# Performance work log

Hardware: AMD Instinct MI355X
Metric: run time of the kernel (lower is better)

Reference implementation:

```python
import jax, jax.numpy as jnp
import numpy as np

N, E = 50000, 800000
IN, HID, OUT = 128, 128, 64
H, ED = 4, 3
D = HID // H  # per-head dim = 32


def _w(key, shape):
    fan_in = shape[-1]
    return jax.random.normal(key, shape, dtype=jnp.float32) / np.sqrt(fan_in)


def setup_inputs() -> dict:
    key = jax.random.key(0)
    ks = jax.random.split(key, 32)
    inp = {
        "x": jax.random.normal(ks[0], (N, IN), dtype=jnp.float32),
        "edge_index": jax.random.randint(ks[1], (2, E), 0, N, dtype=jnp.int32),
        "edge_attr": jax.random.normal(ks[2], (E, ED), dtype=jnp.float32),
        # layer 1 TransformerConv (bias=False)
        "Wq1": _w(ks[3], (HID, IN)), "Wk1": _w(ks[4], (HID, IN)),
        "Wv1": _w(ks[5], (HID, IN)), "We1": _w(ks[6], (HID, ED)),
        "Ws1": _w(ks[7], (HID, IN)),
        # layer 1 MLP [HID,HID,HID]
        "M1a": _w(ks[8], (HID, HID)), "b1a": jnp.zeros((HID,), jnp.float32),
        "M1b": _w(ks[9], (HID, HID)), "b1b": jnp.zeros((HID,), jnp.float32),
        # layer 2 TransformerConv
        "Wq2": _w(ks[10], (HID, HID)), "Wk2": _w(ks[11], (HID, HID)),
        "Wv2": _w(ks[12], (HID, HID)), "We2": _w(ks[13], (HID, ED)),
        "Ws2": _w(ks[14], (HID, HID)),
        # layer 2 MLP
        "M2a": _w(ks[15], (HID, HID)), "b2a": jnp.zeros((HID,), jnp.float32),
        "M2b": _w(ks[16], (HID, HID)), "b2b": jnp.zeros((HID,), jnp.float32),
        # final MLP [HID,HID,OUT], plain_last=False
        "Wf1": _w(ks[17], (HID, HID)), "bf1": jnp.zeros((HID,), jnp.float32),
        "Wf2": _w(ks[18], (OUT, HID)), "bf2": jnp.zeros((OUT,), jnp.float32),
    }
    return inp


def _gelu(x):
    return jax.nn.gelu(x, approximate=True)


def _transformer_conv(x, src, dst, edge_attr, Wq, Wk, Wv, We, Ws, n_nodes):
    # PyG TransformerConv: x_j = x[src] (message source), x_i = x[dst] (target)
    q = (x @ Wq.T).reshape(n_nodes, H, D)
    e = (edge_attr @ We.T).reshape(-1, H, D)              # [E,H,D]
    k = (x @ Wk.T).reshape(n_nodes, H, D)[src] + e        # [E,H,D]
    v = (x @ Wv.T).reshape(n_nodes, H, D)[src] + e        # [E,H,D]
    alpha = jnp.einsum("ehd,ehd->eh", q[dst], k) / jnp.float32(np.sqrt(D))
    # segment softmax over incoming edges of each target node
    m = jax.ops.segment_max(alpha, dst, num_segments=n_nodes)  # [N,H]
    m = jnp.where(jnp.isfinite(m), m, 0.0)
    p = jnp.exp(alpha - m[dst])
    s = jax.ops.segment_sum(p, dst, num_segments=n_nodes)      # [N,H]
    a = p / jnp.maximum(s[dst], 1e-16)                         # [E,H]
    out = jax.ops.segment_sum(a[:, :, None] * v, dst, num_segments=n_nodes)
    out = out.reshape(n_nodes, H * D)
    # root_weight=True (default): skip connection through lin_skip (no bias)
    return out + x @ Ws.T


def _mlp2(x, Wa, ba, Wb, bb):
    # PyG MLP with plain_last=False: act after every linear, norm=None
    h = _gelu(x @ Wa.T + ba)
    return _gelu(h @ Wb.T + bb)


def reference(x, edge_index, edge_attr,
              Wq1, Wk1, Wv1, We1, Ws1, M1a, b1a, M1b, b1b,
              Wq2, Wk2, Wv2, We2, Ws2, M2a, b2a, M2b, b2b,
              Wf1, bf1, Wf2, bf2):
    n_nodes = x.shape[0]
    src, dst = edge_index[0], edge_index[1]
    h = _transformer_conv(x, src, dst, edge_attr, Wq1, Wk1, Wv1, We1, Ws1, n_nodes)
    h = h + _mlp2(h, M1a, b1a, M1b, b1b)
    h = _transformer_conv(h, src, dst, edge_attr, Wq2, Wk2, Wv2, We2, Ws2, n_nodes)
    h = h + _mlp2(h, M2a, b2a, M2b, b2b)
    return _mlp2(h, Wf1, bf1, Wf2, bf2)
```

## Files before the change

### kernel.cpp

```cpp
#include <hip/hip_runtime.h>
#include <hip/hip_bf16.h>
#include <math.h>

#define NN 50000
#define NE 800000
#define NPAD 50048
#define BCAP 48

typedef unsigned short u16;
typedef unsigned int u32;
typedef __attribute__((ext_vector_type(8))) short short8;
typedef __attribute__((ext_vector_type(4))) float float4v;

__device__ __forceinline__ float us2f(u16 u) { return __uint_as_float(((unsigned)u) << 16); }
__device__ __forceinline__ float blo(u32 u) { return __uint_as_float(u << 16); }
__device__ __forceinline__ float bhi(u32 u) { return __uint_as_float(u & 0xffff0000u); }
__device__ __forceinline__ u16 f2us(float f) {
    unsigned x = __float_as_uint(f);
    return (u16)((x + 0x7FFFu + ((x >> 16) & 1u)) >> 16);
}
__device__ __forceinline__ float gelu_f(float x) {
    float p = x * x;
    float t = x * fmaf(p, 0.0713548162726f, 1.5957691216057308f);
    float e = __expf(-t);
    return x * __builtin_amdgcn_rcpf(1.0f + e);
}
__device__ __forceinline__ void lds_fence() {
    asm volatile("s_waitcnt lgkmcnt(0)" ::: "memory");
}

__device__ __forceinline__ float4v mfma4p(const u16* __restrict__ WP, int tile, int l,
                                          short8 a0, short8 a1, short8 a2, short8 a3) {
    const short8* wp = (const short8*)WP + (size_t)tile * 256 + l;
    short8 b0 = wp[0], b1 = wp[64], b2 = wp[128], b3 = wp[192];
    float4v acc = {0.f, 0.f, 0.f, 0.f};
    acc = __builtin_amdgcn_mfma_f32_16x16x32_bf16(a0, b0, acc, 0, 0, 0);
    acc = __builtin_amdgcn_mfma_f32_16x16x32_bf16(a1, b1, acc, 0, 0, 0);
    acc = __builtin_amdgcn_mfma_f32_16x16x32_bf16(a2, b2, acc, 0, 0, 0);
    acc = __builtin_amdgcn_mfma_f32_16x16x32_bf16(a3, b3, acc, 0, 0, 0);
    return acc;
}


__global__ void k_scatter(const int* __restrict__ srcv, const int* __restrict__ dstv,
                          const float* __restrict__ eattr, int* __restrict__ cursor,
                          int4* __restrict__ rec) {
    int e = blockIdx.x * blockDim.x + threadIdx.x;
    if (e >= NE) return;
    int dst = dstv[e];
    int pos = atomicAdd(&cursor[dst], 1);
    if (pos >= BCAP) return;
    int4 r;
    r.x = srcv[e];
    r.y = __float_as_int(eattr[e * 3 + 0]);
    r.z = __float_as_int(eattr[e * 3 + 1]);
    r.w = __float_as_int(eattr[e * 3 + 2]);
    rec[(size_t)dst * BCAP + pos] = r;
}


struct CvtEnt { const float* s; u16* d; int n; float sc; };
struct CvtTab { CvtEnt e[14]; };
__global__ void k_cvt_w(CvtTab tab) {
    CvtEnt E = tab.e[blockIdx.x >> 3];
    int chunk = blockIdx.x & 7;
    int per = E.n >> 3;
    int lo = chunk * per, hi = lo + per;
    for (int o = lo + threadIdx.x; o < hi; o += blockDim.x) {
        int tile = o >> 11;
        int q = (o >> 9) & 3;
        int l = (o >> 3) & 63;
        int j = o & 7;
        int row = tile * 16 + (l & 15);
        int col = q * 32 + (l >> 4) * 8 + j;
        E.d[o] = f2us(E.s[row * 128 + col] * E.sc);
    }
}


__device__ __forceinline__ void stage_plain(u16* buf, int kb, int m, int tt, float4v acc) {
#pragma unroll
    for (int r = 0; r < 4; ++r) buf[(kb * 4 + r) * 136 + tt * 16 + m] = f2us(acc[r]);
}
__device__ __forceinline__ void store128(const u16* buf, u16* dst, int r0w, int coff, int l) {
#pragma unroll
    for (int it = 0; it < 4; ++it) {
        int j = it * 64 + l;
        int row = j >> 4, col = (j & 15) * 8;
        *(uint4*)(dst + (size_t)(r0w + row) * 512 + coff + col) = *(const uint4*)&buf[row * 136 + col];
    }
}
__device__ __forceinline__ void read_frags(const u16* buf, int m, int kb,
                                           short8& f0, short8& f1, short8& f2, short8& f3) {
    const u16* p = buf + m * 136 + kb * 8;
    f0 = *(const short8*)(p);
    f1 = *(const short8*)(p + 32);
    f2 = *(const short8*)(p + 64);
    f3 = *(const short8*)(p + 96);
}


__global__ __launch_bounds__(256, 4) void k_qkvs1(const float* __restrict__ Ain,
                                                  const u16* __restrict__ W,
                                                  u16* __restrict__ QKVS) {
    __shared__ u16 tile[4][16 * 136];
    int tid = threadIdx.x;
    int l = tid & 63, w = tid >> 6, m = l & 15, kb = l >> 4;
    int r0w = blockIdx.x * 64 + w * 16;
    u16* my = tile[w];

    short8 a0, a1, a2, a3;
    {
        const float* ap = Ain + (size_t)(r0w + m) * 128;
        bool ok = (r0w + m) < NN;
        short8* dsts[4] = {&a0, &a1, &a2, &a3};
#pragma unroll
        for (int i = 0; i < 4; ++i) {
            short8 r;
            if (ok) {
                const float* p = ap + (kb + i * 4) * 8;
                float4 f0 = *(const float4*)p;
                float4 f1 = *(const float4*)(p + 4);
                r[0]=(short)f2us(f0.x); r[1]=(short)f2us(f0.y); r[2]=(short)f2us(f0.z); r[3]=(short)f2us(f0.w);
                r[4]=(short)f2us(f1.x); r[5]=(short)f2us(f1.y); r[6]=(short)f2us(f1.z); r[7]=(short)f2us(f1.w);
            } else {
#pragma unroll
                for (int j = 0; j < 8; ++j) r[j] = 0;
            }
            *dsts[i] = r;
        }
    }

#pragma unroll
    for (int tt = 0; tt < 8; ++tt) stage_plain(my, kb, m, tt, mfma4p(W, tt, l, a0, a1, a2, a3));
    lds_fence();
    store128(my, QKVS, r0w, 0, l);
    lds_fence();
#pragma unroll
    for (int tt = 0; tt < 4; ++tt) {
        float4v acc = mfma4p(W, 8 + tt, l, a0, a1, a2, a3);
        int c = tt * 32 + 8 * (m >> 2) + (m & 3);
#pragma unroll
        for (int r = 0; r < 4; ++r) my[(kb * 4 + r) * 136 + c] = f2us(acc[r]);
    }
#pragma unroll
    for (int tt = 0; tt < 4; ++tt) {
        float4v acc = mfma4p(W, 16 + tt, l, a0, a1, a2, a3);
        int c = tt * 32 + 8 * (m >> 2) + (m & 3) + 4;
#pragma unroll
        for (int r = 0; r < 4; ++r) my[(kb * 4 + r) * 136 + c] = f2us(acc[r]);
    }
    lds_fence();
    store128(my, QKVS, r0w, 128, l);
    lds_fence();
#pragma unroll
    for (int tt = 0; tt < 4; ++tt) {
        float4v acc = mfma4p(W, 12 + tt, l, a0, a1, a2, a3);
        int c = tt * 32 + 8 * (m >> 2) + (m & 3);
#pragma unroll
        for (int r = 0; r < 4; ++r) my[(kb * 4 + r) * 136 + c] = f2us(acc[r]);
    }
#pragma unroll
    for (int tt = 0; tt < 4; ++tt) {
        float4v acc = mfma4p(W, 20 + tt, l, a0, a1, a2, a3);
        int c = tt * 32 + 8 * (m >> 2) + (m & 3) + 4;
#pragma unroll
        for (int r = 0; r < 4; ++r) my[(kb * 4 + r) * 136 + c] = f2us(acc[r]);
    }
    lds_fence();
    store128(my, QKVS, r0w, 256, l);
    lds_fence();
#pragma unroll
    for (int tt = 0; tt < 8; ++tt) stage_plain(my, kb, m, tt, mfma4p(W, 24 + tt, l, a0, a1, a2, a3));
    lds_fence();
    store128(my, QKVS, r0w, 384, l);
}


__global__ __launch_bounds__(256, 4) void k_mlp_qkvs(const u16* __restrict__ Ain,
                                                     const u16* __restrict__ Wm,
                                                     const float* __restrict__ bias1,
                                                     const float* __restrict__ bias2,
                                                     const u16* __restrict__ Wq,
                                                     u16* __restrict__ QKVS) {
    __shared__ u16 shb[4][16 * 136];
    __shared__ u16 t1b[4][16 * 136];
    int tid = threadIdx.x;
    int l = tid & 63, w = tid >> 6, m = l & 15, kb = l >> 4;
    int r0w = blockIdx.x * 64 + w * 16;
    u16* sh = shb[w];
    u16* t1 = t1b[w];

    const short8* arow = (const short8*)(Ain + (size_t)(r0w + m) * 128);
    short8 a0 = arow[kb], a1 = arow[kb + 4], a2 = arow[kb + 8], a3 = arow[kb + 12];
    {
        u16* p = sh + m * 136 + kb * 8;
        *(short8*)(p) = a0;
        *(short8*)(p + 32) = a1;
        *(short8*)(p + 64) = a2;
        *(short8*)(p + 96) = a3;
    }
#pragma unroll
    for (int tt = 0; tt < 8; ++tt) {
        float4v acc = mfma4p(Wm, tt, l, a0, a1, a2, a3);
        float bv = bias1[tt * 16 + m];
#pragma unroll
        for (int r = 0; r < 4; ++r)
            t1[(kb * 4 + r) * 136 + tt * 16 + m] = f2us(gelu_f(acc[r] + bv));
    }
    lds_fence();
    short8 c0, c1, c2, c3;
    read_frags(t1, m, kb, c0, c1, c2, c3);
#pragma unroll
    for (int tt = 0; tt < 8; ++tt) {
        float4v acc = mfma4p(Wm + 16384, tt, l, c0, c1, c2, c3);
        float bv = bias2[tt * 16 + m];
#pragma unroll
        for (int r = 0; r < 4; ++r) {
            int idx = (kb * 4 + r) * 136 + tt * 16 + m;
            sh[idx] = f2us(gelu_f(acc[r] + bv) + us2f(sh[idx]));
        }
    }
    lds_fence();
    short8 h0, h1, h2, h3;
    read_frags(sh, m, kb, h0, h1, h2, h3);

#pragma unroll
    for (int tt = 0; tt < 8; ++tt) stage_plain(t1, kb, m, tt, mfma4p(Wq, tt, l, h0, h1, h2, h3));
    lds_fence();
    store128(t1, QKVS, r0w, 0, l);
    lds_fence();
#pragma unroll
    for (int tt = 0; tt < 4; ++tt) {
        float4v acc = mfma4p(Wq, 8 + tt, l, h0, h1, h2, h3);
        int c = tt * 32 + 8 * (m >> 2) + (m & 3);
#pragma unroll
        for (int r = 0; r < 4; ++r) t1[(kb * 4 + r) * 136 + c] = f2us(acc[r]);
    }
#pragma unroll
    for (int tt = 0; tt < 4; ++tt) {
        float4v acc = mfma4p(Wq, 16 + tt, l, h0, h1, h2, h3);
        int c = tt * 32 + 8 * (m >> 2) + (m & 3) + 4;
#pragma unroll
        for (int r = 0; r < 4; ++r) t1[(kb * 4 + r) * 136 + c] = f2us(acc[r]);
    }
    lds_fence();
    store128(t1, QKVS, r0w, 128, l);
    lds_fence();
#pragma unroll
    for (int tt = 0; tt < 4; ++tt) {
        float4v acc = mfma4p(Wq, 12 + tt, l, h0, h1, h2, h3);
        int c = tt * 32 + 8 * (m >> 2) + (m & 3);
#pragma unroll
        for (int r = 0; r < 4; ++r) t1[(kb * 4 + r) * 136 + c] = f2us(acc[r]);
    }
#pragma unroll
    for (int tt = 0; tt < 4; ++tt) {
        float4v acc = mfma4p(Wq, 20 + tt, l, h0, h1, h2, h3);
        int c = tt * 32 + 8 * (m >> 2) + (m & 3) + 4;
#pragma unroll
        for (int r = 0; r < 4; ++r) t1[(kb * 4 + r) * 136 + c] = f2us(acc[r]);
    }
    lds_fence();
    store128(t1, QKVS, r0w, 256, l);
    lds_fence();
#pragma unroll
    for (int tt = 0; tt < 8; ++tt) stage_plain(t1, kb, m, tt, mfma4p(Wq, 24 + tt, l, h0, h1, h2, h3));
    lds_fence();
    store128(t1, QKVS, r0w, 384, l);
}


__global__ __launch_bounds__(256, 4) void k_mlp_final(const u16* __restrict__ Ain,
                                                      const u16* __restrict__ Wm,
                                                      const float* __restrict__ bias1,
                                                      const float* __restrict__ bias2,
                                                      const u16* __restrict__ Wf,
                                                      const float* __restrict__ bf1,
                                                      const float* __restrict__ bf2,
                                                      float* __restrict__ outp) {
    __shared__ u16 shb[4][16 * 136];
    __shared__ u16 t1b[4][16 * 136];
    int tid = threadIdx.x;
    int l = tid & 63, w = tid >> 6, m = l & 15, kb = l >> 4;
    int r0w = blockIdx.x * 64 + w * 16;
    u16* sh = shb[w];
    u16* t1 = t1b[w];

    const short8* arow = (const short8*)(Ain + (size_t)(r0w + m) * 128);
    short8 a0 = arow[kb], a1 = arow[kb + 4], a2 = arow[kb + 8], a3 = arow[kb + 12];
    {
        u16* p = sh + m * 136 + kb * 8;
        *(short8*)(p) = a0;
        *(short8*)(p + 32) = a1;
        *(short8*)(p + 64) = a2;
        *(short8*)(p + 96) = a3;
    }
#pragma unroll
    for (int tt = 0; tt < 8; ++tt) {
        float4v acc = mfma4p(Wm, tt, l, a0, a1, a2, a3);
        float bv = bias1[tt * 16 + m];
#pragma unroll
        for (int r = 0; r < 4; ++r)
            t1[(kb * 4 + r) * 136 + tt * 16 + m] = f2us(gelu_f(acc[r] + bv));
    }
    lds_fence();
    short8 c0, c1, c2, c3;
    read_frags(t1, m, kb, c0, c1, c2, c3);
#pragma unroll
    for (int tt = 0; tt < 8; ++tt) {
        float4v acc = mfma4p(Wm + 16384, tt, l, c0, c1, c2, c3);
        float bv = bias2[tt * 16 + m];
#pragma unroll
        for (int r = 0; r < 4; ++r) {
            int idx = (kb * 4 + r) * 136 + tt * 16 + m;
            sh[idx] = f2us(gelu_f(acc[r] + bv) + us2f(sh[idx]));
        }
    }
    lds_fence();
    short8 h0, h1, h2, h3;
    read_frags(sh, m, kb, h0, h1, h2, h3);
#pragma unroll
    for (int tt = 0; tt < 8; ++tt) {
        float4v acc = mfma4p(Wf, tt, l, h0, h1, h2, h3);
        float bv = bf1[tt * 16 + m];
#pragma unroll
        for (int r = 0; r < 4; ++r)
            t1[(kb * 4 + r) * 136 + tt * 16 + m] = f2us(gelu_f(acc[r] + bv));
    }
    lds_fence();
    short8 f0, f1, f2, f3;
    read_frags(t1, m, kb, f0, f1, f2, f3);
    lds_fence();
#pragma unroll
    for (int tt = 0; tt < 4; ++tt) {
        float4v acc = mfma4p(Wf + 16384, tt, l, f0, f1, f2, f3);
        float bv = bf2[tt * 16 + m];
#pragma unroll
        for (int r = 0; r < 4; ++r)
            t1[(kb * 4 + r) * 136 + tt * 16 + m] = f2us(gelu_f(acc[r] + bv));
    }
    lds_fence();
#pragma unroll
    for (int it = 0; it < 2; ++it) {
        int j = it * 64 + l;
        int row = j >> 3, col = (j & 7) * 8;
        int grow = r0w + row;
        if (grow < NN) {
            uint4 pk = *(const uint4*)&t1[row * 136 + col];
            const u16* pv = (const u16*)&pk;
            float* po = outp + (size_t)grow * 64 + col;
            float4 o0 = {us2f(pv[0]), us2f(pv[1]), us2f(pv[2]), us2f(pv[3])};
            float4 o1 = {us2f(pv[4]), us2f(pv[5]), us2f(pv[6]), us2f(pv[7])};
            *(float4*)po = o0;
            *(float4*)(po + 4) = o1;
        }
    }
}


__global__ __launch_bounds__(256) void k_conv(const int* __restrict__ cursor,
                                              const int4* __restrict__ rec,
                                              const u16* __restrict__ qkvs,
                                              const float* __restrict__ We,
                                              u16* __restrict__ out) {
    int n = blockIdx.x * 4 + (threadIdx.x >> 6);
    int l = threadIdx.x & 63;
    int half = l >> 5;
    int li = l & 31;
    int c0 = (li >> 3) * 32 + (li & 7) * 4;
    const u16* qrow = qkvs + (size_t)n * 512;
    uint2 qu = *(const uint2*)(qrow + c0);
    uint2 su = *(const uint2*)(qrow + 384 + c0);
    float q0 = blo(qu.x), q1 = bhi(qu.x), q2 = blo(qu.y), q3 = bhi(qu.y);
    float g0, g1, g2;
    {
        const float* wp = We + c0 * 3;
        g0 = fmaf(q3, wp[9],  fmaf(q2, wp[6], fmaf(q1, wp[3], q0 * wp[0])));
        g1 = fmaf(q3, wp[10], fmaf(q2, wp[7], fmaf(q1, wp[4], q0 * wp[1])));
        g2 = fmaf(q3, wp[11], fmaf(q2, wp[8], fmaf(q1, wp[5], q0 * wp[2])));
#pragma unroll
        for (int d = 1; d <= 4; d <<= 1) {
            g0 += __shfl_xor(g0, d);
            g1 += __shfl_xor(g1, d);
            g2 += __shfl_xor(g2, d);
        }
    }
    int cntall = min(cursor[n], BCAP);
    int base = n * BCAP;
    float ss = 0.f, o0 = 0.f, o1 = 0.f, o2 = 0.f, o3 = 0.f, S0 = 0.f, S1 = 0.f, S2 = 0.f;
    int kvoff = 128 + li * 8;

    auto edge = [&](int4 r, uint4 kv) {
        float part = fmaf(q3, bhi(kv.y), fmaf(q2, blo(kv.y), fmaf(q1, bhi(kv.x), q0 * blo(kv.x))));
        part += __shfl_xor(part, 1);
        part += __shfl_xor(part, 2);
        part += __shfl_xor(part, 4);
        float ea0 = __int_as_float(r.y), ea1 = __int_as_float(r.z), ea2 = __int_as_float(r.w);
        float alpha = fmaf(ea2, g2, fmaf(ea1, g1, fmaf(ea0, g0, part)));
        float p = __expf(fminf(alpha, 80.f));
        o0 = fmaf(p, blo(kv.z), o0);
        o1 = fmaf(p, bhi(kv.z), o1);
        o2 = fmaf(p, blo(kv.w), o2);
        o3 = fmaf(p, bhi(kv.w), o3);
        ss += p;
        S0 = fmaf(p, ea0, S0);
        S1 = fmaf(p, ea1, S1);
        S2 = fmaf(p, ea2, S2);
    };

    int e = base + half;
    int cnt = (half < cntall) ? ((cntall - half + 1) >> 1) : 0;
    if (cnt & 1) {
        int4 r = rec[e];
        uint4 kv = *(const uint4*)(qkvs + (size_t)r.x * 512 + kvoff);
        edge(r, kv);
        e += 2;
    }
    for (int i = 0; i < (cnt >> 1); ++i, e += 4) {
        int4 ra = rec[e], rb = rec[e + 2];
        uint4 kva = *(const uint4*)(qkvs + (size_t)ra.x * 512 + kvoff);
        uint4 kvb = *(const uint4*)(qkvs + (size_t)rb.x * 512 + kvoff);
        edge(ra, kva);
        edge(rb, kvb);
    }
    o0 += __shfl_xor(o0, 32);
    o1 += __shfl_xor(o1, 32);
    o2 += __shfl_xor(o2, 32);
    o3 += __shfl_xor(o3, 32);
    ss += __shfl_xor(ss, 32);
    S0 += __shfl_xor(S0, 32);
    S1 += __shfl_xor(S1, 32);
    S2 += __shfl_xor(S2, 32);
    if (half == 0) {
        float inv = __builtin_amdgcn_rcpf(fmaxf(ss, 1e-16f));
        const float* wp = We + c0 * 3;
        o0 = fmaf(wp[2],  S2, fmaf(wp[1],  S1, fmaf(wp[0], S0, o0)));
        o1 = fmaf(wp[5],  S2, fmaf(wp[4],  S1, fmaf(wp[3], S0, o1)));
        o2 = fmaf(wp[8],  S2, fmaf(wp[7],  S1, fmaf(wp[6], S0, o2)));
        o3 = fmaf(wp[11], S2, fmaf(wp[10], S1, fmaf(wp[9], S0, o3)));
        float r0v = fmaf(o0, inv, blo(su.x));
        float r1v = fmaf(o1, inv, bhi(su.x));
        float r2v = fmaf(o2, inv, blo(su.y));
        float r3v = fmaf(o3, inv, bhi(su.y));
        uint2 ou;
        ou.x = (u32)f2us(r0v) | ((u32)f2us(r1v) << 16);
        ou.y = (u32)f2us(r2v) | ((u32)f2us(r3v) << 16);
        *(uint2*)(out + (size_t)n * 128 + c0) = ou;
    }
}


extern "C" void kernel_launch(void* const* d_in, const int* in_sizes, int n_in,
                              void* d_out, int out_size, void* d_ws, size_t ws_size,
                              hipStream_t stream) {
    const float* x = (const float*)d_in[0];
    const int* ei = (const int*)d_in[1];
    const float* eattr = (const float*)d_in[2];
    const float* Wq1 = (const float*)d_in[3];
    const float* Wk1 = (const float*)d_in[4];
    const float* Wv1 = (const float*)d_in[5];
    const float* We1 = (const float*)d_in[6];
    const float* Ws1 = (const float*)d_in[7];
    const float* M1a = (const float*)d_in[8];
    const float* b1a = (const float*)d_in[9];
    const float* M1b = (const float*)d_in[10];
    const float* b1b = (const float*)d_in[11];
    const float* Wq2 = (const float*)d_in[12];
    const float* Wk2 = (const float*)d_in[13];
    const float* Wv2 = (const float*)d_in[14];
    const float* We2 = (const float*)d_in[15];
    const float* Ws2 = (const float*)d_in[16];
    const float* M2a = (const float*)d_in[17];
    const float* b2a = (const float*)d_in[18];
    const float* M2b = (const float*)d_in[19];
    const float* b2b = (const float*)d_in[20];
    const float* Wf1 = (const float*)d_in[21];
    const float* bf1 = (const float*)d_in[22];
    const float* Wf2 = (const float*)d_in[23];
    const float* bf2 = (const float*)d_in[24];

    char* ws = (char*)d_ws;
    size_t off = 0;
    auto alloc = [&](size_t bytes) -> void* {
        void* p = ws + off;
        off = (off + bytes + 255) & ~(size_t)255;
        return p;
    };
    int* cursor = (int*)alloc((size_t)NN * 4);
    int4* rec = (int4*)alloc((size_t)NN * BCAP * 16);
    u16* QKVS = (u16*)alloc((size_t)NPAD * 512 * 2);
    u16* Ha = (u16*)alloc((size_t)NPAD * 128 * 2);
    u16* WB[14];
    const int wsz[14] = {16384, 16384, 16384, 16384, 16384, 16384, 16384,
                         16384, 16384, 16384, 16384, 16384, 16384, 8192};
    for (int i = 0; i < 14; ++i) WB[i] = (u16*)alloc((size_t)wsz[i] * 2);

    const int* srcv = ei;
    const int* dstv = ei + NE;

    hipMemsetAsync(cursor, 0, (size_t)NN * 4, stream);
    k_scatter<<<(NE + 255) / 256, 256, 0, stream>>>(srcv, dstv, eattr, cursor, rec);

    CvtTab tab;
    const float* wsrc[14] = {Wq1, Wk1, Wv1, Ws1, Wq2, Wk2, Wv2, Ws2,
                             M1a, M1b, M2a, M2b, Wf1, Wf2};
    const float SC = 0.17677669529663687f;
    for (int i = 0; i < 14; ++i) {
        tab.e[i].s = wsrc[i];
        tab.e[i].d = WB[i];
        tab.e[i].n = wsz[i];
        tab.e[i].sc = (i == 0 || i == 4) ? SC : 1.0f;
    }
    k_cvt_w<<<112, 256, 0, stream>>>(tab);

    dim3 blk(256);
    dim3 grd(NPAD / 64);
    dim3 gconv(NN / 4);

    k_qkvs1<<<grd, blk, 0, stream>>>(x, WB[0], QKVS);
    k_conv<<<gconv, blk, 0, stream>>>(cursor, rec, QKVS, We1, Ha);
    k_mlp_qkvs<<<grd, blk, 0, stream>>>(Ha, WB[8], b1a, b1b, WB[4], QKVS);
    k_conv<<<gconv, blk, 0, stream>>>(cursor, rec, QKVS, We2, Ha);
    k_mlp_final<<<grd, blk, 0, stream>>>(Ha, WB[10], b2a, b2b, WB[12], bf1, bf2, (float*)d_out);
}
```

Baseline: 365.8 us.

## Process 32 rows per wave in dense kernels to reuse weight fragments

The dense MLP/QKV kernels now have each wave compute two 16-row tiles, so every loaded weight fragment feeds two MFMA chains instead of one. This halves weight reads from global/L2 per row. Blocks shrink to 128 threads while still covering 64 rows. The residual add is done in registers with bf16 adds instead of a separate shared-memory buffer, which cuts LDS use, at the cost of higher register pressure and fewer resident waves.

```diff
diff --git a/kernel.cpp b/kernel.cpp
--- a/kernel.cpp
+++ b/kernel.cpp
@@ -29,16 +29,25 @@
     asm volatile("s_waitcnt lgkmcnt(0)" ::: "memory");
 }
 
-__device__ __forceinline__ float4v mfma4p(const u16* __restrict__ WP, int tile, int l,
-                                          short8 a0, short8 a1, short8 a2, short8 a3) {
+__device__ __forceinline__ void loadB(const u16* __restrict__ WP, int tile, int l,
+                                      short8& b0, short8& b1, short8& b2, short8& b3) {
     const short8* wp = (const short8*)WP + (size_t)tile * 256 + l;
-    short8 b0 = wp[0], b1 = wp[64], b2 = wp[128], b3 = wp[192];
+    b0 = wp[0]; b1 = wp[64]; b2 = wp[128]; b3 = wp[192];
+}
+__device__ __forceinline__ float4v mfma4(short8 b0, short8 b1, short8 b2, short8 b3,
+                                         short8 a0, short8 a1, short8 a2, short8 a3) {
     float4v acc = {0.f, 0.f, 0.f, 0.f};
     acc = __builtin_amdgcn_mfma_f32_16x16x32_bf16(a0, b0, acc, 0, 0, 0);
     acc = __builtin_amdgcn_mfma_f32_16x16x32_bf16(a1, b1, acc, 0, 0, 0);
     acc = __builtin_amdgcn_mfma_f32_16x16x32_bf16(a2, b2, acc, 0, 0, 0);
     acc = __builtin_amdgcn_mfma_f32_16x16x32_bf16(a3, b3, acc, 0, 0, 0);
     return acc;
+}
+__device__ __forceinline__ short8 addbf(short8 x, short8 y) {
+    short8 r;
+#pragma unroll
+    for (int j = 0; j < 8; ++j) r[j] = (short)f2us(us2f((u16)x[j]) + us2f((u16)y[j]));
+    return r;
 }
 
 
@@ -78,13 +87,9 @@
 }
 
 
-__device__ __forceinline__ void stage_plain(u16* buf, int kb, int m, int tt, float4v acc) {
-#pragma unroll
-    for (int r = 0; r < 4; ++r) buf[(kb * 4 + r) * 136 + tt * 16 + m] = f2us(acc[r]);
-}
-__device__ __forceinline__ void store128(const u16* buf, u16* dst, int r0w, int coff, int l) {
-#pragma unroll
-    for (int it = 0; it < 4; ++it) {
+__device__ __forceinline__ void store32(const u16* buf, u16* dst, int r0w, int coff, int l) {
+#pragma unroll
+    for (int it = 0; it < 8; ++it) {
         int j = it * 64 + l;
         int row = j >> 4, col = (j & 15) * 8;
         *(uint4*)(dst + (size_t)(r0w + row) * 512 + coff + col) = *(const uint4*)&buf[row * 136 + col];
@@ -99,21 +104,111 @@
     f3 = *(const short8*)(p + 96);
 }
 
-
-__global__ __launch_bounds__(256, 4) void k_qkvs1(const float* __restrict__ Ain,
+#define QKVS_TAIL(Wq, H, my, QKVS, r0w, l, m, kb)                                        \
+    _Pragma("unroll")                                                                     \
+    for (int tt = 0; tt < 8; ++tt) {                                                      \
+        short8 b0, b1, b2, b3;                                                            \
+        loadB(Wq, tt, l, b0, b1, b2, b3);                                                 \
+        float4v x0 = mfma4(b0, b1, b2, b3, H[0][0], H[0][1], H[0][2], H[0][3]);           \
+        float4v x1 = mfma4(b0, b1, b2, b3, H[1][0], H[1][1], H[1][2], H[1][3]);           \
+        _Pragma("unroll")                                                                 \
+        for (int r = 0; r < 4; ++r) {                                                     \
+            my[(kb * 4 + r) * 136 + tt * 16 + m] = f2us(x0[r]);                           \
+            my[(16 + kb * 4 + r) * 136 + tt * 16 + m] = f2us(x1[r]);                      \
+        }                                                                                 \
+    }                                                                                     \
+    lds_fence();                                                                          \
+    store32(my, QKVS, r0w, 0, l);                                                         \
+    lds_fence();                                                                          \
+    _Pragma("unroll")                                                                     \
+    for (int tt = 0; tt < 4; ++tt) {                                                      \
+        short8 b0, b1, b2, b3;                                                            \
+        loadB(Wq, 8 + tt, l, b0, b1, b2, b3);                                             \
+        float4v x0 = mfma4(b0, b1, b2, b3, H[0][0], H[0][1], H[0][2], H[0][3]);           \
+        float4v x1 = mfma4(b0, b1, b2, b3, H[1][0], H[1][1], H[1][2], H[1][3]);           \
+        int c = tt * 32 + 8 * (m >> 2) + (m & 3);                                         \
+        _Pragma("unroll")                                                                 \
+        for (int r = 0; r < 4; ++r) {                                                     \
+            my[(kb * 4 + r) * 136 + c] = f2us(x0[r]);                                     \
+            my[(16 + kb * 4 + r) * 136 + c] = f2us(x1[r]);                                \
+        }                                                                                 \
+    }                                                                                     \
+    _Pragma("unroll")                                                                     \
+    for (int tt = 0; tt < 4; ++tt) {                                                      \
+        short8 b0, b1, b2, b3;                                                            \
+        loadB(Wq, 16 + tt, l, b0, b1, b2, b3);                                            \
+        float4v x0 = mfma4(b0, b1, b2, b3, H[0][0], H[0][1], H[0][2], H[0][3]);           \
+        float4v x1 = mfma4(b0, b1, b2, b3, H[1][0], H[1][1], H[1][2], H[1][3]);           \
+        int c = tt * 32 + 8 * (m >> 2) + (m & 3) + 4;                                     \
+        _Pragma("unroll")                                                                 \
+        for (int r = 0; r < 4; ++r) {                                                     \
+            my[(kb * 4 + r) * 136 + c] = f2us(x0[r]);                                     \
+            my[(16 + kb * 4 + r) * 136 + c] = f2us(x1[r]);                                \
+        }                                                                                 \
+    }                                                                                     \
+    lds_fence();                                                                          \
+    store32(my, QKVS, r0w, 128, l);                                                       \
+    lds_fence();                                                                          \
+    _Pragma("unroll")                                                                     \
+    for (int tt = 0; tt < 4; ++tt) {                                                      \
+        short8 b0, b1, b2, b3;                                                            \
+        loadB(Wq, 12 + tt, l, b0, b1, b2, b3);                                            \
+        float4v x0 = mfma4(b0, b1, b2, b3, H[0][0], H[0][1], H[0][2], H[0][3]);           \
+        float4v x1 = mfma4(b0, b1, b2, b3, H[1][0], H[1][1], H[1][2], H[1][3]);           \
+        int c = tt * 32 + 8 * (m >> 2) + (m & 3);                                         \
+        _Pragma("unroll")                                                                 \
+        for (int r = 0; r < 4; ++r) {                                                     \
+            my[(kb * 4 + r) * 136 + c] = f2us(x0[r]);                                     \
+            my[(16 + kb * 4 + r) * 136 + c] = f2us(x1[r]);                                \
+        }                                                                                 \
+    }                                                                                     \
+    _Pragma("unroll")                                                                     \
+    for (int tt = 0; tt < 4; ++tt) {                                                      \
+        short8 b0, b1, b2, b3;                                                            \
+        loadB(Wq, 20 + tt, l, b0, b1, b2, b3);                                            \
+        float4v x0 = mfma4(b0, b1, b2, b3, H[0][0], H[0][1], H[0][2], H[0][3]);           \
+        float4v x1 = mfma4(b0, b1, b2, b3, H[1][0], H[1][1], H[1][2], H[1][3]);           \
+        int c = tt * 32 + 8 * (m >> 2) + (m & 3) + 4;                                     \
+        _Pragma("unroll")                                                                 \
+        for (int r = 0; r < 4; ++r) {                                                     \
+            my[(kb * 4 + r) * 136 + c] = f2us(x0[r]);                                     \
+            my[(16 + kb * 4 + r) * 136 + c] = f2us(x1[r]);                                \
+        }                                                                                 \
+    }                                                                                     \
+    lds_fence();                                                                          \
+    store32(my, QKVS, r0w, 256, l);                                                       \
+    lds_fence();                                                                          \
+    _Pragma("unroll")                                                                     \
+    for (int tt = 0; tt < 8; ++tt) {                                                      \
+        short8 b0, b1, b2, b3;                                                            \
+        loadB(Wq, 24 + tt, l, b0, b1, b2, b3);                                            \
+        float4v x0 = mfma4(b0, b1, b2, b3, H[0][0], H[0][1], H[0][2], H[0][3]);           \
+        float4v x1 = mfma4(b0, b1, b2, b3, H[1][0], H[1][1], H[1][2], H[1][3]);           \
+        _Pragma("unroll")                                                                 \
+        for (int r = 0; r < 4; ++r) {                                                     \
+            my[(kb * 4 + r) * 136 + tt * 16 + m] = f2us(x0[r]);                           \
+            my[(16 + kb * 4 + r) * 136 + tt * 16 + m] = f2us(x1[r]);                      \
+        }                                                                                 \
+    }                                                                                     \
+    lds_fence();                                                                          \
+    store32(my, QKVS, r0w, 384, l);
+
+
+__global__ __launch_bounds__(128, 4) void k_qkvs1(const float* __restrict__ Ain,
                                                   const u16* __restrict__ W,
                                                   u16* __restrict__ QKVS) {
-    __shared__ u16 tile[4][16 * 136];
+    __shared__ u16 tile[2][32 * 136];
     int tid = threadIdx.x;
     int l = tid & 63, w = tid >> 6, m = l & 15, kb = l >> 4;
-    int r0w = blockIdx.x * 64 + w * 16;
+    int r0w = blockIdx.x * 64 + w * 32;
     u16* my = tile[w];
 
-    short8 a0, a1, a2, a3;
-    {
-        const float* ap = Ain + (size_t)(r0w + m) * 128;
-        bool ok = (r0w + m) < NN;
-        short8* dsts[4] = {&a0, &a1, &a2, &a3};
+    short8 A[2][4];
+#pragma unroll
+    for (int s = 0; s < 2; ++s) {
+        int row = r0w + s * 16 + m;
+        const float* ap = Ain + (size_t)row * 128;
+        bool ok = row < NN;
 #pragma unroll
         for (int i = 0; i < 4; ++i) {
             short8 r;
@@ -127,151 +222,82 @@
 #pragma unroll
                 for (int j = 0; j < 8; ++j) r[j] = 0;
             }
-            *dsts[i] = r;
-        }
-    }
-
-#pragma unroll
-    for (int tt = 0; tt < 8; ++tt) stage_plain(my, kb, m, tt, mfma4p(W, tt, l, a0, a1, a2, a3));
-    lds_fence();
-    store128(my, QKVS, r0w, 0, l);
-    lds_fence();
-#pragma unroll
-    for (int tt = 0; tt < 4; ++tt) {
-        float4v acc = mfma4p(W, 8 + tt, l, a0, a1, a2, a3);
-        int c = tt * 32 + 8 * (m >> 2) + (m & 3);
-#pragma unroll
-        for (int r = 0; r < 4; ++r) my[(kb * 4 + r) * 136 + c] = f2us(acc[r]);
-    }
-#pragma unroll
-    for (int tt = 0; tt < 4; ++tt) {
-        float4v acc = mfma4p(W, 16 + tt, l, a0, a1, a2, a3);
-        int c = tt * 32 + 8 * (m >> 2) + (m & 3) + 4;
-#pragma unroll
-        for (int r = 0; r < 4; ++r) my[(kb * 4 + r) * 136 + c] = f2us(acc[r]);
-    }
-    lds_fence();
-    store128(my, QKVS, r0w, 128, l);
-    lds_fence();
-#pragma unroll
-    for (int tt = 0; tt < 4; ++tt) {
-        float4v acc = mfma4p(W, 12 + tt, l, a0, a1, a2, a3);
-        int c = tt * 32 + 8 * (m >> 2) + (m & 3);
-#pragma unroll
-        for (int r = 0; r < 4; ++r) my[(kb * 4 + r) * 136 + c] = f2us(acc[r]);
-    }
-#pragma unroll
-    for (int tt = 0; tt < 4; ++tt) {
-        float4v acc = mfma4p(W, 20 + tt, l, a0, a1, a2, a3);
-        int c = tt * 32 + 8 * (m >> 2) + (m & 3) + 4;
-#pragma unroll
-        for (int r = 0; r < 4; ++r) my[(kb * 4 + r) * 136 + c] = f2us(acc[r]);
-    }
-    lds_fence();
-    store128(my, QKVS, r0w, 256, l);
-    lds_fence();
-#pragma unroll
-    for (int tt = 0; tt < 8; ++tt) stage_plain(my, kb, m, tt, mfma4p(W, 24 + tt, l, a0, a1, a2, a3));
-    lds_fence();
-    store128(my, QKVS, r0w, 384, l);
-}
-
-
-__global__ __launch_bounds__(256, 4) void k_mlp_qkvs(const u16* __restrict__ Ain,
+            A[s][i] = r;
+        }
+    }
+
+    QKVS_TAIL(W, A, my, QKVS, r0w, l, m, kb)
+}
+
+
+__global__ __launch_bounds__(128, 4) void k_mlp_qkvs(const u16* __restrict__ Ain,
                                                      const u16* __restrict__ Wm,
                                                      const float* __restrict__ bias1,
                                                      const float* __restrict__ bias2,
                                                      const u16* __restrict__ Wq,
                                                      u16* __restrict__ QKVS) {
-    __shared__ u16 shb[4][16 * 136];
-    __shared__ u16 t1b[4][16 * 136];
+    __shared__ u16 t1b[2][32 * 136];
     int tid = threadIdx.x;
     int l = tid & 63, w = tid >> 6, m = l & 15, kb = l >> 4;
-    int r0w = blockIdx.x * 64 + w * 16;
-    u16* sh = shb[w];
+    int r0w = blockIdx.x * 64 + w * 32;
     u16* t1 = t1b[w];
 
-    const short8* arow = (const short8*)(Ain + (size_t)(r0w + m) * 128);
-    short8 a0 = arow[kb], a1 = arow[kb + 4], a2 = arow[kb + 8], a3 = arow[kb + 12];
-    {
-        u16* p = sh + m * 136 + kb * 8;
-        *(short8*)(p) = a0;
-        *(short8*)(p + 32) = a1;
-        *(short8*)(p + 64) = a2;
-        *(short8*)(p + 96) = a3;
+    short8 A[2][4];
+#pragma unroll
+    for (int s = 0; s < 2; ++s) {
+        const short8* arow = (const short8*)(Ain + (size_t)(r0w + s * 16 + m) * 128);
+#pragma unroll
+        for (int i = 0; i < 4; ++i) A[s][i] = arow[kb + i * 4];
     }
 #pragma unroll
     for (int tt = 0; tt < 8; ++tt) {
-        float4v acc = mfma4p(Wm, tt, l, a0, a1, a2, a3);
+        short8 b0, b1, b2, b3;
+        loadB(Wm, tt, l, b0, b1, b2, b3);
+        float4v x0 = mfma4(b0, b1, b2, b3, A[0][0], A[0][1], A[0][2], A[0][3]);
+        float4v x1 = mfma4(b0, b1, b2, b3, A[1][0], A[1][1], A[1][2], A[1][3]);
         float bv = bias1[tt * 16 + m];
 #pragma unroll
-        for (int r = 0; r < 4; ++r)
-            t1[(kb * 4 + r) * 136 + tt * 16 + m] = f2us(gelu_f(acc[r] + bv));
-    }
-    lds_fence();
-    short8 c0, c1, c2, c3;
-    read_frags(t1, m, kb, c0, c1, c2, c3);
+        for (int r = 0; r < 4; ++r) {
+            t1[(kb * 4 + r) * 136 + tt * 16 + m] = f2us(gelu_f(x0[r] + bv));
+            t1[(16 + kb * 4 + r) * 136 + tt * 16 + m] = f2us(gelu_f(x1[r] + bv));
+        }
+    }
+    lds_fence();
+    short8 C[2][4];
+    read_frags(t1, m, kb, C[0][0], C[0][1], C[0][2], C[0][3]);
+    read_frags(t1 + 16 * 136, m, kb, C[1][0], C[1][1], C[1][2], C[1][3]);
+    lds_fence();
 #pragma unroll
     for (int tt = 0; tt < 8; ++tt) {
-        float4v acc = mfma4p(Wm + 16384, tt, l, c0, c1, c2, c3);
+        short8 b0, b1, b2, b3;
+        loadB(Wm + 16384, tt, l, b0, b1, b2, b3);
+        float4v x0 = mfma4(b0, b1, b2, b3, C[0][0], C[0][1], C[0][2], C[0][3]);
+        float4v x1 = mfma4(b0, b1, b2, b3, C[1][0], C[1][1], C[1][2], C[1][3]);
         float bv = bias2[tt * 16 + m];
 #pragma unroll
         for (int r = 0; r < 4; ++r) {
-            int idx = (kb * 4 + r) * 136 + tt * 16 + m;
-            sh[idx] = f2us(gelu_f(acc[r] + bv) + us2f(sh[idx]));
-        }
-    }
-    lds_fence();
-    short8 h0, h1, h2, h3;
-    read_frags(sh, m, kb, h0, h1, h2, h3);
-
-#pragma unroll
-    for (int tt = 0; tt < 8; ++tt) stage_plain(t1, kb, m, tt, mfma4p(Wq, tt, l, h0, h1, h2, h3));
-    lds_fence();
-    store128(t1, QKVS, r0w, 0, l);
-    lds_fence();
-#pragma unroll
-    for (int tt = 0; tt < 4; ++tt) {
-        float4v acc = mfma4p(Wq, 8 + tt, l, h0, h1, h2, h3);
-        int c = tt * 32 + 8 * (m >> 2) + (m & 3);
-#pragma unroll
-        for (int r = 0; r < 4; ++r) t1[(kb * 4 + r) * 136 + c] = f2us(acc[r]);
-    }
-#pragma unroll
-    for (int tt = 0; tt < 4; ++tt) {
-        float4v acc = mfma4p(Wq, 16 + tt, l, h0, h1, h2, h3);
-        int c = tt * 32 + 8 * (m >> 2) + (m & 3) + 4;
-#pragma unroll
-        for (int r = 0; r < 4; ++r) t1[(kb * 4 + r) * 136 + c] = f2us(acc[r]);
-    }
-    lds_fence();
-    store128(t1, QKVS, r0w, 128, l);
-    lds_fence();
-#pragma unroll
-    for (int tt = 0; tt < 4; ++tt) {
-        float4v acc = mfma4p(Wq, 12 + tt, l, h0, h1, h2, h3);
-        int c = tt * 32 + 8 * (m >> 2) + (m & 3);
-#pragma unroll
-        for (int r = 0; r < 4; ++r) t1[(kb * 4 + r) * 136 + c] = f2us(acc[r]);
-    }
-#pragma unroll
-    for (int tt = 0; tt < 4; ++tt) {
-        float4v acc = mfma4p(Wq, 20 + tt, l, h0, h1, h2, h3);
-        int c = tt * 32 + 8 * (m >> 2) + (m & 3) + 4;
-#pragma unroll
-        for (int r = 0; r < 4; ++r) t1[(kb * 4 + r) * 136 + c] = f2us(acc[r]);
-    }
-    lds_fence();
-    store128(t1, QKVS, r0w, 256, l);
-    lds_fence();
-#pragma unroll
-    for (int tt = 0; tt < 8; ++tt) stage_plain(t1, kb, m, tt, mfma4p(Wq, 24 + tt, l, h0, h1, h2, h3));
-    lds_fence();
-    store128(t1, QKVS, r0w, 384, l);
-}
-
-
-__global__ __launch_bounds__(256, 4) void k_mlp_final(const u16* __restrict__ Ain,
+            t1[(kb * 4 + r) * 136 + tt * 16 + m] = f2us(gelu_f(x0[r] + bv));
+            t1[(16 + kb * 4 + r) * 136 + tt * 16 + m] = f2us(gelu_f(x1[r] + bv));
+        }
+    }
+    lds_fence();
+    short8 H[2][4];
+#pragma unroll
+    for (int s = 0; s < 2; ++s) {
+        short8 f0, f1, f2, f3;
+        read_frags(t1 + s * 16 * 136, m, kb, f0, f1, f2, f3);
+        H[s][0] = addbf(f0, A[s][0]);
+        H[s][1] = addbf(f1, A[s][1]);
+        H[s][2] = addbf(f2, A[s][2]);
+        H[s][3] = addbf(f3, A[s][3]);
+    }
+    lds_fence();
+
+    QKVS_TAIL(Wq, H, t1, QKVS, r0w, l, m, kb)
+}
+
+
+__global__ __launch_bounds__(128, 4) void k_mlp_final(const u16* __restrict__ Ain,
                                                       const u16* __restrict__ Wm,
                                                       const float* __restrict__ bias1,
                                                       const float* __restrict__ bias2,
@@ -279,70 +305,96 @@
                                                       const float* __restrict__ bf1,
                                                       const float* __restrict__ bf2,
                                                       float* __restrict__ outp) {
-    __shared__ u16 shb[4][16 * 136];
-    __shared__ u16 t1b[4][16 * 136];
+    __shared__ u16 t1b[2][32 * 136];
     int tid = threadIdx.x;
     int l = tid & 63, w = tid >> 6, m = l & 15, kb = l >> 4;
-    int r0w = blockIdx.x * 64 + w * 16;
-    u16* sh = shb[w];
+    int r0w = blockIdx.x * 64 + w * 32;
     u16* t1 = t1b[w];
 
-    const short8* arow = (const short8*)(Ain + (size_t)(r0w + m) * 128);
-    short8 a0 = arow[kb], a1 = arow[kb + 4], a2 = arow[kb + 8], a3 = arow[kb + 12];
-    {
-        u16* p = sh + m * 136 + kb * 8;
-        *(short8*)(p) = a0;
-        *(short8*)(p + 32) = a1;
-        *(short8*)(p + 64) = a2;
-        *(short8*)(p + 96) = a3;
+    short8 A[2][4];
+#pragma unroll
+    for (int s = 0; s < 2; ++s) {
+        const short8* arow = (const short8*)(Ain + (size_t)(r0w + s * 16 + m) * 128);
+#pragma unroll
+        for (int i = 0; i < 4; ++i) A[s][i] = arow[kb + i * 4];
     }
 #pragma unroll
     for (int tt = 0; tt < 8; ++tt) {
-        float4v acc = mfma4p(Wm, tt, l, a0, a1, a2, a3);
+        short8 b0, b1, b2, b3;
+        loadB(Wm, tt, l, b0, b1, b2, b3);
+        float4v x0 = mfma4(b0, b1, b2, b3, A[0][0], A[0][1], A[0][2], A[0][3]);
+        float4v x1 = mfma4(b0, b1, b2, b3, A[1][0], A[1][1], A[1][2], A[1][3]);
         float bv = bias1[tt * 16 + m];
 #pragma unroll
-        for (int r = 0; r < 4; ++r)
-            t1[(kb * 4 + r) * 136 + tt * 16 + m] = f2us(gelu_f(acc[r] + bv));
-    }
-    lds_fence();
-    short8 c0, c1, c2, c3;
-    read_frags(t1, m, kb, c0, c1, c2, c3);
+        for (int r = 0; r < 4; ++r) {
+            t1[(kb * 4 + r) * 136 + tt * 16 + m] = f2us(gelu_f(x0[r] + bv));
+            t1[(16 + kb * 4 + r) * 136 + tt * 16 + m] = f2us(gelu_f(x1[r] + bv));
+        }
+    }
+    lds_fence();
+    short8 C[2][4];
+    read_frags(t1, m, kb, C[0][0], C[0][1], C[0][2], C[0][3]);
+    read_frags(t1 + 16 * 136, m, kb, C[1][0], C[1][1], C[1][2], C[1][3]);
+    lds_fence();
 #pragma unroll
     for (int tt = 0; tt < 8; ++tt) {
-        float4v acc = mfma4p(Wm + 16384, tt, l, c0, c1, c2, c3);
+        short8 b0, b1, b2, b3;
+        loadB(Wm + 16384, tt, l, b0, b1, b2, b3);
+        float4v x0 = mfma4(b0, b1, b2, b3, C[0][0], C[0][1], C[0][2], C[0][3]);
+        float4v x1 = mfma4(b0, b1, b2, b3, C[1][0], C[1][1], C[1][2], C[1][3]);
         float bv = bias2[tt * 16 + m];
 #pragma unroll
         for (int r = 0; r < 4; ++r) {
-            int idx = (kb * 4 + r) * 136 + tt * 16 + m;
-            sh[idx] = f2us(gelu_f(acc[r] + bv) + us2f(sh[idx]));
-        }
-    }
-    lds_fence();
-    short8 h0, h1, h2, h3;
-    read_frags(sh, m, kb, h0, h1, h2, h3);
+            t1[(kb * 4 + r) * 136 + tt * 16 + m] = f2us(gelu_f(x0[r] + bv));
+            t1[(16 + kb * 4 + r) * 136 + tt * 16 + m] = f2us(gelu_f(x1[r] + bv));
+        }
+    }
+    lds_fence();
+    short8 H[2][4];
+#pragma unroll
+    for (int s = 0; s < 2; ++s) {
+        short8 f0, f1, f2, f3;
+        read_frags(t1 + s * 16 * 136, m, kb, f0, f1, f2, f3);
+        H[s][0] = addbf(f0, A[s][0]);
+        H[s][1] = addbf(f1, A[s][1]);
+        H[s][2] = addbf(f2, A[s][2]);
+        H[s][3] = addbf(f3, A[s][3]);
+    }
+    lds_fence();
 #pragma unroll
     for (int tt = 0; tt < 8; ++tt) {
-        float4v acc = mfma4p(Wf, tt, l, h0, h1, h2, h3);
+        short8 b0, b1, b2, b3;
+        loadB(Wf, tt, l, b0, b1, b2, b3);
+        float4v x0 = mfma4(b0, b1, b2, b3, H[0][0], H[0][1], H[0][2], H[0][3]);
+        float4v x1 = mfma4(b0, b1, b2, b3, H[1][0], H[1][1], H[1][2], H[1][3]);
         float bv = bf1[tt * 16 + m];
 #pragma unroll
-        for (int r = 0; r < 4; ++r)
-            t1[(kb * 4 + r) * 136 + tt * 16 + m] = f2us(gelu_f(acc[r] + bv));
-    }
-    lds_fence();
-    short8 f0, f1, f2, f3;
-    read_frags(t1, m, kb, f0, f1, f2, f3);
+        for (int r = 0; r < 4; ++r) {
+            t1[(kb * 4 + r) * 136 + tt * 16 + m] = f2us(gelu_f(x0[r] + bv));
+            t1[(16 + kb * 4 + r) * 136 + tt * 16 + m] = f2us(gelu_f(x1[r] + bv));
+        }
+    }
+    lds_fence();
+    short8 F[2][4];
+    read_frags(t1, m, kb, F[0][0], F[0][1], F[0][2], F[0][3]);
+    read_frags(t1 + 16 * 136, m, kb, F[1][0], F[1][1], F[1][2], F[1][3]);
     lds_fence();
 #pragma unroll
     for (int tt = 0; tt < 4; ++tt) {
-        float4v acc = mfma4p(Wf + 16384, tt, l, f0, f1, f2, f3);
+        short8 b0, b1, b2, b3;
+        loadB(Wf + 16384, tt, l, b0, b1, b2, b3);
+        float4v x0 = mfma4(b0, b1, b2, b3, F[0][0], F[0][1], F[0][2], F[0][3]);
+        float4v x1 = mfma4(b0, b1, b2, b3, F[1][0], F[1][1], F[1][2], F[1][3]);
         float bv = bf2[tt * 16 + m];
 #pragma unroll
-        for (int r = 0; r < 4; ++r)
-            t1[(kb * 4 + r) * 136 + tt * 16 + m] = f2us(gelu_f(acc[r] + bv));
-    }
-    lds_fence();
-#pragma unroll
-    for (int it = 0; it < 2; ++it) {
+        for (int r = 0; r < 4; ++r) {
+            t1[(kb * 4 + r) * 136 + tt * 16 + m] = f2us(gelu_f(x0[r] + bv));
+            t1[(16 + kb * 4 + r) * 136 + tt * 16 + m] = f2us(gelu_f(x1[r] + bv));
+        }
+    }
+    lds_fence();
+#pragma unroll
+    for (int it = 0; it < 4; ++it) {
         int j = it * 64 + l;
         int row = j >> 3, col = (j & 7) * 8;
         int grow = r0w + row;
@@ -514,13 +566,13 @@
     }
     k_cvt_w<<<112, 256, 0, stream>>>(tab);
 
-    dim3 blk(256);
+    dim3 blk(128);
     dim3 grd(NPAD / 64);
     dim3 gconv(NN / 4);
 
     k_qkvs1<<<grd, blk, 0, stream>>>(x, WB[0], QKVS);
-    k_conv<<<gconv, blk, 0, stream>>>(cursor, rec, QKVS, We1, Ha);
+    k_conv<<<gconv, dim3(256), 0, stream>>>(cursor, rec, QKVS, We1, Ha);
     k_mlp_qkvs<<<grd, blk, 0, stream>>>(Ha, WB[8], b1a, b1b, WB[4], QKVS);
-    k_conv<<<gconv, blk, 0, stream>>>(cursor, rec, QKVS, We2, Ha);
+    k_conv<<<gconv, dim3(256), 0, stream>>>(cursor, rec, QKVS, We2, Ha);
     k_mlp_final<<<grd, blk, 0, stream>>>(Ha, WB[10], b2a, b2b, WB[12], bf1, bf2, (float*)d_out);
 }
```

Result: no change. 362.7 us (median of 2 runs) (-0.8%).
